# Kernel optimization log

Hardware: AMD Instinct MI355X
Metric: run time of the kernel (lower is better)

The kernel has to match this reference:

```python
import jax, jax.numpy as jnp
import numpy as np

N_SEQ, N_RES, C_M, C_Z, C, N_HEAD = 256, 256, 256, 128, 32, 8
EPS = 1e-5


def layernorm(x, w, b):
    mu = jnp.mean(x, axis=-1, keepdims=True)
    var = jnp.mean((x - mu) ** 2, axis=-1, keepdims=True)
    return (x - mu) * jax.lax.rsqrt(var + EPS) * w + b


def setup_inputs() -> dict:
    key = jax.random.key(0)
    ks = jax.random.split(key, 12)
    s = 0.02
    return {
        "m": jax.random.normal(ks[0], (N_SEQ, N_RES, C_M), jnp.float32),
        "z": jax.random.normal(ks[1], (N_RES, N_RES, C_Z), jnp.float32),
        "ln_m_w": jnp.ones((C_M,), jnp.float32),
        "ln_m_b": jnp.zeros((C_M,), jnp.float32),
        "ln_z_w": jnp.ones((C_Z,), jnp.float32),
        "ln_z_b": jnp.zeros((C_Z,), jnp.float32),
        "Wz": jax.random.normal(ks[2], (C_Z, N_HEAD), jnp.float32) * s,   # pair bias proj, no bias
        "Wq": jax.random.normal(ks[3], (C_M, N_HEAD * C), jnp.float32) * s,
        "Wk": jax.random.normal(ks[4], (C_M, N_HEAD * C), jnp.float32) * s,
        "Wv": jax.random.normal(ks[5], (C_M, N_HEAD * C), jnp.float32) * s,
        "Wg": jax.random.normal(ks[6], (C_M, N_HEAD * C), jnp.float32) * s,
        "bg": jnp.zeros((N_HEAD * C,), jnp.float32),
        "Wo": jax.random.normal(ks[7], (N_HEAD * C, C_M), jnp.float32) * s,
        "bo": jnp.zeros((C_M,), jnp.float32),
    }


def reference(m, z, ln_m_w, ln_m_b, ln_z_w, ln_z_b, Wz, Wq, Wk, Wv, Wg, bg, Wo, bo):
    # LayerNorm on msa and pair reps
    mn = layernorm(m, ln_m_w, ln_m_b)                       # (S, R, c_m)
    b = layernorm(z, ln_z_w, ln_z_b) @ Wz                    # (R, R, H)
    b = jnp.moveaxis(b, -1, -3)                              # (H, R, R)

    def proj(W):  # (S, R, H, C) -> (S, H, R, C)
        return (mn @ W).reshape(N_SEQ, N_RES, N_HEAD, C).transpose(0, 2, 1, 3)

    q = proj(Wq) / jnp.sqrt(jnp.float32(C))
    k = proj(Wk)
    v = proj(Wv)

    scores = jnp.einsum("shqc,shkc->shqk", q, k) + b         # bias broadcasts over S
    a = jax.nn.softmax(scores, axis=-1)
    o = jnp.einsum("shqk,shkc->shqc", a, v)                  # (S, H, R, C)
    o = o.transpose(0, 2, 1, 3).reshape(N_SEQ, N_RES, N_HEAD * C)

    g = jax.nn.sigmoid(mn @ Wg + bg)                          # gating
    return (g * o) @ Wo + bo                                  # (S, R, c_m)
```

## Files before the change

kernel.cpp:

```cpp
#include <hip/hip_runtime.h>
#include <stdint.h>

#define NSEQ 256
#define NRES 256
#define CM   256
#define CZ   128
#define CH   32
#define NHEAD 8
#define EPSF 1e-5f

typedef __bf16 bf16x8 __attribute__((ext_vector_type(8)));
typedef float  f32x4  __attribute__((ext_vector_type(4)));
typedef float  f32x16 __attribute__((ext_vector_type(16)));

__device__ __forceinline__ ushort f2bf(float f) {
    union { float f; uint32_t u; } v; v.f = f;
    uint32_t r = (v.u + 0x7FFFu + ((v.u >> 16) & 1u)) >> 16;
    return (ushort)r;
}
__device__ __forceinline__ float bf2f(ushort h) {
    union { uint32_t u; float f; } v; v.u = ((uint32_t)h) << 16;
    return v.f;
}
__device__ __forceinline__ float bfl(uint32_t u) {
    union { uint32_t x; float f; } v; v.x = u << 16; return v.f;
}
__device__ __forceinline__ float bfh(uint32_t u) {
    union { uint32_t x; float f; } v; v.x = u & 0xffff0000u; return v.f;
}
__device__ __forceinline__ unsigned int cvt_pk_bf16(float lo, float hi_) {
    unsigned int r;
    asm("v_cvt_pk_bf16_f32 %0, %1, %2" : "=v"(r) : "v"(lo), "v"(hi_));
    return r;
}

__device__ __forceinline__ void gload16(const void* g, void* l) {
    __builtin_amdgcn_global_load_lds(
        (const __attribute__((address_space(1))) void*)g,
        (__attribute__((address_space(3))) void*)l,
        16, 0, 0);
}

__global__ void prep_weights_kernel(const float* __restrict__ Wq,
                                    const float* __restrict__ Wk,
                                    const float* __restrict__ Wv,
                                    const float* __restrict__ Wg,
                                    const float* __restrict__ Wo,
                                    ushort* __restrict__ Wt,
                                    ushort* __restrict__ WoT) {
    int n = blockIdx.x;
    int k = threadIdx.x;
    if (n < 1024) {
        int nn = n & 255;
        const float* src;
        float scale = 1.0f;
        if      (n < 256) { src = Wq; scale = 0.17677669529663687f; }
        else if (n < 512) { src = Wk; }
        else if (n < 768) { src = Wv; }
        else              { src = Wg; }
        Wt[n * 256 + k] = f2bf(src[k * 256 + nn] * scale);
    } else {
        int nn = n - 1024;
        WoT[nn * 256 + k] = f2bf(Wo[k * 256 + nn]);
    }
}

__global__ __launch_bounds__(256) void ln_m_kernel(const float* __restrict__ m,
                                                   const float* __restrict__ w,
                                                   const float* __restrict__ b,
                                                   ushort* __restrict__ mn) {
    int gw   = (blockIdx.x * blockDim.x + threadIdx.x) >> 6;
    int lane = threadIdx.x & 63;
    const float* row = m + (size_t)gw * 256;
    float4 x = *(const float4*)(row + lane * 4);
    float s  = x.x + x.y + x.z + x.w;
    float sq = x.x * x.x + x.y * x.y + x.z * x.z + x.w * x.w;
#pragma unroll
    for (int off = 32; off; off >>= 1) {
        s  += __shfl_xor(s, off, 64);
        sq += __shfl_xor(sq, off, 64);
    }
    float mu  = s * (1.0f / 256.0f);
    float var = sq * (1.0f / 256.0f) - mu * mu;
    float rs  = rsqrtf(var + EPSF);
    float4 wv = *(const float4*)(w + lane * 4);
    float4 bv = *(const float4*)(b + lane * 4);
    ushort4 o;
    o.x = f2bf((x.x - mu) * rs * wv.x + bv.x);
    o.y = f2bf((x.y - mu) * rs * wv.y + bv.y);
    o.z = f2bf((x.z - mu) * rs * wv.z + bv.z);
    o.w = f2bf((x.w - mu) * rs * wv.w + bv.w);
    *(ushort4*)(mn + (size_t)gw * 256 + lane * 4) = o;
}

__global__ __launch_bounds__(256) void ln_z_bias_kernel(const float* __restrict__ z,
                                                        const float* __restrict__ w,
                                                        const float* __restrict__ b,
                                                        const float* __restrict__ Wz,
                                                        ushort* __restrict__ biasb) {
    int gw   = (blockIdx.x * blockDim.x + threadIdx.x) >> 6;
    int lane = threadIdx.x & 63;
    float wz0[8], wz1[8];
#pragma unroll
    for (int h = 0; h < 8; ++h) {
        wz0[h] = Wz[(2 * lane) * 8 + h];
        wz1[h] = Wz[(2 * lane + 1) * 8 + h];
    }
    float w0 = w[2 * lane], w1 = w[2 * lane + 1];
    float b0 = b[2 * lane], b1 = b[2 * lane + 1];
    for (int row = gw; row < 65536; row += 8192) {
        float2 x = *(const float2*)(z + (size_t)row * 128 + 2 * lane);
        float s = x.x + x.y, sq = x.x * x.x + x.y * x.y;
#pragma unroll
        for (int off = 32; off; off >>= 1) {
            s  += __shfl_xor(s, off, 64);
            sq += __shfl_xor(sq, off, 64);
        }
        float mu = s * (1.0f / 128.0f);
        float rs = rsqrtf(sq * (1.0f / 128.0f) - mu * mu + EPSF);
        float z0 = (x.x - mu) * rs * w0 + b0;
        float z1 = (x.y - mu) * rs * w1 + b1;
        float acc[8];
#pragma unroll
        for (int h = 0; h < 8; ++h) acc[h] = z0 * wz0[h] + z1 * wz1[h];
#pragma unroll
        for (int h = 0; h < 8; ++h)
#pragma unroll
            for (int off = 32; off; off >>= 1) acc[h] += __shfl_xor(acc[h], off, 64);
        if (lane < 8) {
            int jc = row & 31;
            int posv = ((jc & 4) << 2) | ((jc & 24) >> 1) | (jc & 3);
            biasb[lane * 65536 + (row & ~31) + posv] = f2bf(acc[lane]);
        }
    }
}

__global__ __launch_bounds__(256) void proj_gemm_kernel(const ushort* __restrict__ mn,
                                                        const ushort* __restrict__ Wt,
                                                        const float* __restrict__ bg,
                                                        ushort* __restrict__ Q,
                                                        ushort* __restrict__ K,
                                                        ushort* __restrict__ Vt,
                                                        ushort* __restrict__ G) {
    __shared__ ushort SH[32768];
    int bid = blockIdx.x;
    int wid = ((bid & 7) << 9) | (bid >> 3);
    int by = wid >> 3, bx = wid & 7;
    int m0 = by << 7, n0 = bx << 7;
    int t = threadIdx.x, lane = t & 63, w = t >> 6;
    int l15 = lane & 15, l4 = lane >> 4;
    int wr = w >> 1, wc = w & 1;

    int srow  = t >> 3;
    int scolh = (((lane & 7) ^ ((lane >> 3) & 7)) << 3);
    const ushort* Ag = mn + (size_t)(m0 + srow) * 256 + scolh;
    const ushort* Bg = Wt + (size_t)(n0 + srow) * 256 + scolh;

    auto stage = [&](int kt) {
        int k0 = kt << 6;
        int bufo = (kt & 1) << 14;
#pragma unroll
        for (int i = 0; i < 4; ++i) {
            gload16(Ag + (size_t)(i * 32) * 256 + k0, &SH[bufo + t * 8 + i * 2048]);
            gload16(Bg + (size_t)(i * 32) * 256 + k0, &SH[bufo + 8192 + t * 8 + i * 2048]);
        }
    };

    f32x4 acc[4][4] = {};
    stage(0);

    for (int kt = 0; kt < 4; ++kt) {
        __syncthreads();
        if (kt < 3) stage(kt + 1);
        int bufo = (kt & 1) << 14;
#pragma unroll
        for (int ks = 0; ks < 2; ++ks) {
            int xr = ks * 4 + l4;
            bf16x8 af[4], bfr[4];
#pragma unroll
            for (int mi = 0; mi < 4; ++mi) {
                int row = wr * 64 + mi * 16 + l15;
                af[mi] = *(const bf16x8*)&SH[bufo + row * 64 + ((xr ^ (l15 & 7)) << 3)];
            }
#pragma unroll
            for (int ni = 0; ni < 4; ++ni) {
                int row = wc * 64 + ni * 16 + l15;
                bfr[ni] = *(const bf16x8*)&SH[bufo + 8192 + row * 64 + ((xr ^ (l15 & 7)) << 3)];
            }
#pragma unroll
            for (int mi = 0; mi < 4; ++mi)
#pragma unroll
                for (int ni = 0; ni < 4; ++ni)
                    acc[mi][ni] = __builtin_amdgcn_mfma_f32_16x16x32_bf16(af[mi], bfr[ni], acc[mi][ni], 0, 0, 0);
        }
    }

    __syncthreads();

    int region = bx >> 1;
    int ss = m0 >> 8;

    if (region == 2) {
        int rbase = (m0 & 255) + wr * 64 + l4 * 4;
#pragma unroll
        for (int ni = 0; ni < 4; ++ni) {
            int nn = (n0 & 255) + wc * 64 + ni * 16 + l15;
            int h = nn >> 5, c = nn & 31;
#pragma unroll
            for (int mi = 0; mi < 4; ++mi) {
                int rr = rbase + mi * 16;
                ushort4 pv;
                pv.x = f2bf(acc[mi][ni][0]); pv.y = f2bf(acc[mi][ni][1]);
                pv.z = f2bf(acc[mi][ni][2]); pv.w = f2bf(acc[mi][ni][3]);
                *(ushort4*)&Vt[((size_t)(ss * 8 + h) * 32 + c) * 256 + rr] = pv;
            }
        }
    } else {
        ushort* E = SH + w * 1152;
        int base_nn = (bx & 1) * 128 + wc * 64;
        int rloc = lane >> 2, seg = lane & 3;
#pragma unroll
        for (int mi = 0; mi < 4; ++mi) {
            if (region == 3) {
#pragma unroll
                for (int ni = 0; ni < 4; ++ni) {
                    float bgv = bg[base_nn + ni * 16 + l15];
#pragma unroll
                    for (int r = 0; r < 4; ++r) {
                        float x = acc[mi][ni][r] + bgv;
                        E[(l4 * 4 + r) * 72 + ni * 16 + l15] =
                            f2bf(1.0f / (1.0f + __expf(-x)));
                    }
                }
            } else {
#pragma unroll
                for (int ni = 0; ni < 4; ++ni)
#pragma unroll
                    for (int r = 0; r < 4; ++r)
                        E[(l4 * 4 + r) * 72 + ni * 16 + l15] = f2bf(acc[mi][ni][r]);
            }
            uint4 v0 = *(const uint4*)&E[rloc * 72 + seg * 16];
            uint4 v1 = *(const uint4*)&E[rloc * 72 + seg * 16 + 8];
            int rr  = (m0 & 255) + wr * 64 + mi * 16 + rloc;
            int nn0 = base_nn + seg * 16;
            int h0 = nn0 >> 5, c0 = nn0 & 31;
            int nn1 = nn0 + 8;
            int h1 = nn1 >> 5, c1 = nn1 & 31;
            if (region <= 1) {
                ushort* dst = (region == 0) ? Q : K;
                *(uint4*)&dst[(size_t)(ss * 8 + h0) * 8192 + rr * 32 + c0] = v0;
                *(uint4*)&dst[(size_t)(ss * 8 + h1) * 8192 + rr * 32 + c1] = v1;
            } else {
                *(uint4*)&G[((size_t)h0 << 21) + (ss << 13) + (rr << 5) + c0] = v0;
                *(uint4*)&G[((size_t)h1 << 21) + (ss << 13) + (rr << 5) + c1] = v1;
            }
        }
    }
}

__global__ __launch_bounds__(512, 4) void attn_kernel(const ushort* __restrict__ Q,
                                                      const ushort* __restrict__ K,
                                                      const ushort* __restrict__ Vt,
                                                      const ushort* __restrict__ G,
                                                      const ushort* __restrict__ biasb,
                                                      ushort* __restrict__ GO) {
    __shared__ ushort smem[32768];
    const int t = threadIdx.x;
    const int lane = t & 63, w = t >> 6;
    const int l31 = lane & 31, hi = lane >> 5;
    const int h = blockIdx.x & 7, s0 = blockIdx.x >> 3;
    const int q0 = w * 32;

    auto stage = [&](int i) {
        size_t shb = (size_t)((i * 64 + s0) * 8 + h) * 8192;
        const ushort* Kg = K + shb;
        const ushort* Vg = Vt + shb;
        int bufo = (i & 1) * 16384;
#pragma unroll
        for (int rd = 0; rd < 2; ++rd) {
            int g1 = rd * 512 + t;
            int kk = g1 >> 2;
            int lgk = (g1 & 3) ^ ((kk >> 1) & 3);
            gload16(Kg + kk * 32 + lgk * 8, &smem[bufo + g1 * 8]);
            int cc = g1 >> 5;
            int lgv = (g1 & 31) ^ (cc & 7);
            gload16(Vg + cc * 256 + lgv * 8, &smem[bufo + 8192 + g1 * 8]);
        }
    };

    stage(0);

    for (int i = 0; i < 4; ++i) {
        __syncthreads();
        if (i < 3) stage(i + 1);

        const int s = i * 64 + s0;
        const size_t shb = (size_t)(s * 8 + h) * 8192;
        const int bufo = (i & 1) * 16384;

        bf16x8 qf0 = *(const bf16x8*)&Q[shb + (size_t)(q0 + l31) * 32 + hi * 8];
        bf16x8 qf1 = *(const bf16x8*)&Q[shb + (size_t)(q0 + l31) * 32 + 16 + hi * 8];

        const ushort* bp = biasb + (size_t)h * 65536 + (size_t)(q0 + l31) * 256 + hi * 16;
        const int vbase = bufo + 8192 + l31 * 256;
        const int vswz = l31 & 7;

        float l_run = 0.f;
        f32x16 oa = {}, ob = {};

#pragma unroll 2
        for (int kt = 0; kt < 8; ++kt) {
            uint4 b0 = *(const uint4*)&bp[kt * 32];
            uint4 b1 = *(const uint4*)&bp[kt * 32 + 8];
            f32x16 sa;
            sa[0]  = bfl(b0.x); sa[1]  = bfh(b0.x);
            sa[2]  = bfl(b0.y); sa[3]  = bfh(b0.y);
            sa[4]  = bfl(b0.z); sa[5]  = bfh(b0.z);
            sa[6]  = bfl(b0.w); sa[7]  = bfh(b0.w);
            sa[8]  = bfl(b1.x); sa[9]  = bfh(b1.x);
            sa[10] = bfl(b1.y); sa[11] = bfh(b1.y);
            sa[12] = bfl(b1.z); sa[13] = bfh(b1.z);
            sa[14] = bfl(b1.w); sa[15] = bfh(b1.w);

            int krow = kt * 32 + l31;
            int swz = (krow >> 1) & 3;
            int rb = bufo + krow * 32;
            bf16x8 kf0 = *(const bf16x8*)&smem[rb + ((hi ^ swz) << 3)];
            bf16x8 kf1 = *(const bf16x8*)&smem[rb + (((2 + hi) ^ swz) << 3)];
            sa = __builtin_amdgcn_mfma_f32_32x32x16_bf16(kf0, qf0, sa, 0, 0, 0);
            sa = __builtin_amdgcn_mfma_f32_32x32x16_bf16(kf1, qf1, sa, 0, 0, 0);

            float ls0 = 0.f, ls1 = 0.f;
#pragma unroll
            for (int r = 0; r < 16; r += 2) {
                float p0 = __expf(sa[r]);
                float p1 = __expf(sa[r + 1]);
                sa[r] = p0; sa[r + 1] = p1;
                ls0 += p0; ls1 += p1;
            }
            l_run += ls0 + ls1;

            unsigned int w0[4], w1[4];
#pragma unroll
            for (int mm = 0; mm < 4; ++mm) {
                w0[mm] = cvt_pk_bf16(sa[4 * mm + 0], sa[4 * mm + 1]);
                w1[mm] = cvt_pk_bf16(sa[4 * mm + 2], sa[4 * mm + 3]);
            }
#pragma unroll
            for (int hh = 0; hh < 2; ++hh) {
                unsigned int F0 = w0[2 * hh], H0 = w0[2 * hh + 1];
                unsigned int F1 = w1[2 * hh], H1 = w1[2 * hh + 1];
                asm("v_permlane32_swap_b32 %0, %1" : "+v"(F0), "+v"(H0));
                asm("v_permlane32_swap_b32 %0, %1" : "+v"(F1), "+v"(H1));
                uint4 fw = make_uint4(F0, F1, H0, H1);
                bf16x8 pf = *(bf16x8*)&fw;
                int g = kt * 4 + hh * 2 + hi;
                bf16x8 vf = *(const bf16x8*)&smem[vbase + ((g ^ vswz) << 3)];
                if (hh) ob = __builtin_amdgcn_mfma_f32_32x32x16_bf16(vf, pf, ob, 0, 0, 0);
                else    oa = __builtin_amdgcn_mfma_f32_32x32x16_bf16(vf, pf, oa, 0, 0, 0);
            }
        }

        l_run += __shfl_xor(l_run, 32, 64);
        float rinv = 1.0f / l_run;

        const size_t grow = ((size_t)h << 21) + ((size_t)s << 13) + ((q0 + l31) << 5) + hi * 4;
#pragma unroll
        for (int g = 0; g < 4; ++g) {
            ushort4 gv = *(const ushort4*)&G[grow + g * 8];
            float o0 = (oa[4 * g + 0] + ob[4 * g + 0]) * rinv * bf2f(gv.x);
            float o1 = (oa[4 * g + 1] + ob[4 * g + 1]) * rinv * bf2f(gv.y);
            float o2 = (oa[4 * g + 2] + ob[4 * g + 2]) * rinv * bf2f(gv.z);
            float o3 = (oa[4 * g + 3] + ob[4 * g + 3]) * rinv * bf2f(gv.w);
            ushort4 ov;
            ov.x = f2bf(o0); ov.y = f2bf(o1); ov.z = f2bf(o2); ov.w = f2bf(o3);
            *(ushort4*)&GO[grow + g * 8] = ov;
        }
    }
}

__global__ __launch_bounds__(256) void out_gemm_kernel(const ushort* __restrict__ GO,
                                                       const ushort* __restrict__ WoT,
                                                       const float* __restrict__ bo,
                                                       float* __restrict__ out) {
    __shared__ ushort SH[32768];
    int bid = blockIdx.x;
    int wid = ((bid & 7) << 7) | (bid >> 3);
    int by = wid >> 1, bx = wid & 1;
    int m0 = by << 7, n0 = bx << 7;
    int t = threadIdx.x, lane = t & 63, w = t >> 6;
    int l15 = lane & 15, l4 = lane >> 4;
    int wr = w >> 1, wc = w & 1;

    int srow  = t >> 3;
    int scolh = (((lane & 7) ^ ((lane >> 3) & 7)) << 3);
    const ushort* Ag = GO + ((size_t)(scolh >> 5) << 21) + ((size_t)(m0 + srow) << 5) + (scolh & 31);
    const ushort* Bg = WoT + (size_t)(n0 + srow) * 256 + scolh;

    auto stage = [&](int kt) {
        int k0 = kt << 6;
        int bufo = (kt & 1) << 14;
#pragma unroll
        for (int i = 0; i < 4; ++i) {
            gload16(Ag + ((size_t)kt << 22) + (i << 10), &SH[bufo + t * 8 + i * 2048]);
            gload16(Bg + (size_t)(i * 32) * 256 + k0, &SH[bufo + 8192 + t * 8 + i * 2048]);
        }
    };

    f32x4 acc[4][4] = {};
    stage(0);

    for (int kt = 0; kt < 4; ++kt) {
        __syncthreads();
        if (kt < 3) stage(kt + 1);
        int bufo = (kt & 1) << 14;
#pragma unroll
        for (int ks = 0; ks < 2; ++ks) {
            int xr = ks * 4 + l4;
            bf16x8 af[4], bfr[4];
#pragma unroll
            for (int mi = 0; mi < 4; ++mi) {
                int row = wr * 64 + mi * 16 + l15;
                af[mi] = *(const bf16x8*)&SH[bufo + row * 64 + ((xr ^ (l15 & 7)) << 3)];
            }
#pragma unroll
            for (int ni = 0; ni < 4; ++ni) {
                int row = wc * 64 + ni * 16 + l15;
                bfr[ni] = *(const bf16x8*)&SH[bufo + 8192 + row * 64 + ((xr ^ (l15 & 7)) << 3)];
            }
#pragma unroll
            for (int mi = 0; mi < 4; ++mi)
#pragma unroll
                for (int ni = 0; ni < 4; ++ni)
                    acc[mi][ni] = __builtin_amdgcn_mfma_f32_16x16x32_bf16(af[mi], bfr[ni], acc[mi][ni], 0, 0, 0);
        }
    }

    int crow0 = m0 + wr * 64 + l4 * 4;
#pragma unroll
    for (int ni = 0; ni < 4; ++ni) {
        int col = n0 + wc * 64 + ni * 16 + l15;
        float bov = bo[col];
#pragma unroll
        for (int mi = 0; mi < 4; ++mi)
#pragma unroll
            for (int r = 0; r < 4; ++r)
                out[(size_t)(crow0 + mi * 16 + r) * 256 + col] = acc[mi][ni][r] + bov;
    }
}

extern "C" void kernel_launch(void* const* d_in, const int* in_sizes, int n_in,
                              void* d_out, int out_size, void* d_ws, size_t ws_size,
                              hipStream_t stream) {
    const float* m      = (const float*)d_in[0];
    const float* z      = (const float*)d_in[1];
    const float* ln_m_w = (const float*)d_in[2];
    const float* ln_m_b = (const float*)d_in[3];
    const float* ln_z_w = (const float*)d_in[4];
    const float* ln_z_b = (const float*)d_in[5];
    const float* Wz     = (const float*)d_in[6];
    const float* Wq     = (const float*)d_in[7];
    const float* Wk     = (const float*)d_in[8];
    const float* Wv     = (const float*)d_in[9];
    const float* Wg     = (const float*)d_in[10];
    const float* bg     = (const float*)d_in[11];
    const float* Wo     = (const float*)d_in[12];
    const float* bo     = (const float*)d_in[13];
    float* out = (float*)d_out;

    char* ws = (char*)d_ws;
    ushort* Wt    = (ushort*)(ws + 0);
    ushort* WoT   = (ushort*)(ws + 524288);
    ushort* biasb = (ushort*)(ws + 655360);
    ushort* mn    = (ushort*)(ws + 2752512);
    ushort* GO    = mn;
    ushort* Q     = (ushort*)(ws + 36306944);
    ushort* K     = (ushort*)(ws + 69861376);
    ushort* Vt    = (ushort*)(ws + 103415808);
    ushort* G     = (ushort*)(ws + 136970240);

    prep_weights_kernel<<<1280, 256, 0, stream>>>(Wq, Wk, Wv, Wg, Wo, Wt, WoT);
    ln_m_kernel<<<16384, 256, 0, stream>>>(m, ln_m_w, ln_m_b, mn);
    ln_z_bias_kernel<<<2048, 256, 0, stream>>>(z, ln_z_w, ln_z_b, Wz, biasb);
    proj_gemm_kernel<<<4096, 256, 0, stream>>>(mn, Wt, bg, Q, K, Vt, G);
    attn_kernel<<<512, 512, 0, stream>>>(Q, K, Vt, G, biasb, GO);
    out_gemm_kernel<<<1024, 256, 0, stream>>>(GO, WoT, bo, out);
}
```

Before: 227.6 us.

## Merge preprocessing kernels, use butterfly bias reduction, shrink GEMM K-tile for occupancy

Three preprocessing kernels (weight transpose, m LayerNorm, z LayerNorm plus bias projection) are merged into one launch that dispatches on block index, which removes launch gaps. The 8-head bias reduction now uses a transpose-style butterfly shuffle, so each lane ends up holding one head, instead of 8 full cross-lane reductions. The projection GEMM K-tile is halved from 64 to 32, which halves LDS per block and adds a launch bound of 4 for occupancy. In exchange it needs twice as many barrier iterations, and the LDS swizzle and head index mapping are new and could introduce errors.

```diff
diff --git a/kernel.cpp b/kernel.cpp
--- a/kernel.cpp
+++ b/kernel.cpp
@@ -41,108 +41,127 @@
         16, 0, 0);
 }
 
-__global__ void prep_weights_kernel(const float* __restrict__ Wq,
-                                    const float* __restrict__ Wk,
-                                    const float* __restrict__ Wv,
-                                    const float* __restrict__ Wg,
-                                    const float* __restrict__ Wo,
-                                    ushort* __restrict__ Wt,
-                                    ushort* __restrict__ WoT) {
-    int n = blockIdx.x;
-    int k = threadIdx.x;
-    if (n < 1024) {
-        int nn = n & 255;
-        const float* src;
-        float scale = 1.0f;
-        if      (n < 256) { src = Wq; scale = 0.17677669529663687f; }
-        else if (n < 512) { src = Wk; }
-        else if (n < 768) { src = Wv; }
-        else              { src = Wg; }
-        Wt[n * 256 + k] = f2bf(src[k * 256 + nn] * scale);
-    } else {
-        int nn = n - 1024;
-        WoT[nn * 256 + k] = f2bf(Wo[k * 256 + nn]);
-    }
-}
-
-__global__ __launch_bounds__(256) void ln_m_kernel(const float* __restrict__ m,
-                                                   const float* __restrict__ w,
-                                                   const float* __restrict__ b,
-                                                   ushort* __restrict__ mn) {
-    int gw   = (blockIdx.x * blockDim.x + threadIdx.x) >> 6;
-    int lane = threadIdx.x & 63;
-    const float* row = m + (size_t)gw * 256;
-    float4 x = *(const float4*)(row + lane * 4);
-    float s  = x.x + x.y + x.z + x.w;
-    float sq = x.x * x.x + x.y * x.y + x.z * x.z + x.w * x.w;
-#pragma unroll
-    for (int off = 32; off; off >>= 1) {
-        s  += __shfl_xor(s, off, 64);
-        sq += __shfl_xor(sq, off, 64);
-    }
-    float mu  = s * (1.0f / 256.0f);
-    float var = sq * (1.0f / 256.0f) - mu * mu;
-    float rs  = rsqrtf(var + EPSF);
-    float4 wv = *(const float4*)(w + lane * 4);
-    float4 bv = *(const float4*)(b + lane * 4);
-    ushort4 o;
-    o.x = f2bf((x.x - mu) * rs * wv.x + bv.x);
-    o.y = f2bf((x.y - mu) * rs * wv.y + bv.y);
-    o.z = f2bf((x.z - mu) * rs * wv.z + bv.z);
-    o.w = f2bf((x.w - mu) * rs * wv.w + bv.w);
-    *(ushort4*)(mn + (size_t)gw * 256 + lane * 4) = o;
-}
-
-__global__ __launch_bounds__(256) void ln_z_bias_kernel(const float* __restrict__ z,
-                                                        const float* __restrict__ w,
-                                                        const float* __restrict__ b,
-                                                        const float* __restrict__ Wz,
-                                                        ushort* __restrict__ biasb) {
-    int gw   = (blockIdx.x * blockDim.x + threadIdx.x) >> 6;
-    int lane = threadIdx.x & 63;
-    float wz0[8], wz1[8];
-#pragma unroll
-    for (int h = 0; h < 8; ++h) {
-        wz0[h] = Wz[(2 * lane) * 8 + h];
-        wz1[h] = Wz[(2 * lane + 1) * 8 + h];
-    }
-    float w0 = w[2 * lane], w1 = w[2 * lane + 1];
-    float b0 = b[2 * lane], b1 = b[2 * lane + 1];
-    for (int row = gw; row < 65536; row += 8192) {
-        float2 x = *(const float2*)(z + (size_t)row * 128 + 2 * lane);
-        float s = x.x + x.y, sq = x.x * x.x + x.y * x.y;
+__global__ __launch_bounds__(256) void pre_kernel(const float* __restrict__ m,
+                                                  const float* __restrict__ ln_m_w,
+                                                  const float* __restrict__ ln_m_b,
+                                                  const float* __restrict__ z,
+                                                  const float* __restrict__ ln_z_w,
+                                                  const float* __restrict__ ln_z_b,
+                                                  const float* __restrict__ Wz,
+                                                  const float* __restrict__ Wq,
+                                                  const float* __restrict__ Wk,
+                                                  const float* __restrict__ Wv,
+                                                  const float* __restrict__ Wg,
+                                                  const float* __restrict__ Wo,
+                                                  ushort* __restrict__ mn,
+                                                  ushort* __restrict__ biasb,
+                                                  ushort* __restrict__ Wt,
+                                                  ushort* __restrict__ WoT) {
+    int b = blockIdx.x;
+    int t = threadIdx.x;
+    int lane = t & 63;
+
+    if (b < 16384) {
+        int gw = (b * 256 + t) >> 6;
+        const float* row = m + (size_t)gw * 256;
+        float4 x = *(const float4*)(row + lane * 4);
+        float s  = x.x + x.y + x.z + x.w;
+        float sq = x.x * x.x + x.y * x.y + x.z * x.z + x.w * x.w;
 #pragma unroll
         for (int off = 32; off; off >>= 1) {
             s  += __shfl_xor(s, off, 64);
             sq += __shfl_xor(sq, off, 64);
         }
-        float mu = s * (1.0f / 128.0f);
-        float rs = rsqrtf(sq * (1.0f / 128.0f) - mu * mu + EPSF);
-        float z0 = (x.x - mu) * rs * w0 + b0;
-        float z1 = (x.y - mu) * rs * w1 + b1;
-        float acc[8];
-#pragma unroll
-        for (int h = 0; h < 8; ++h) acc[h] = z0 * wz0[h] + z1 * wz1[h];
-#pragma unroll
-        for (int h = 0; h < 8; ++h)
-#pragma unroll
-            for (int off = 32; off; off >>= 1) acc[h] += __shfl_xor(acc[h], off, 64);
-        if (lane < 8) {
-            int jc = row & 31;
-            int posv = ((jc & 4) << 2) | ((jc & 24) >> 1) | (jc & 3);
-            biasb[lane * 65536 + (row & ~31) + posv] = f2bf(acc[lane]);
+        float mu  = s * (1.0f / 256.0f);
+        float var = sq * (1.0f / 256.0f) - mu * mu;
+        float rs  = rsqrtf(var + EPSF);
+        float4 wv = *(const float4*)(ln_m_w + lane * 4);
+        float4 bv = *(const float4*)(ln_m_b + lane * 4);
+        ushort4 o;
+        o.x = f2bf((x.x - mu) * rs * wv.x + bv.x);
+        o.y = f2bf((x.y - mu) * rs * wv.y + bv.y);
+        o.z = f2bf((x.z - mu) * rs * wv.z + bv.z);
+        o.w = f2bf((x.w - mu) * rs * wv.w + bv.w);
+        *(ushort4*)(mn + (size_t)gw * 256 + lane * 4) = o;
+    } else if (b < 18432) {
+        int gw = ((b - 16384) * 256 + t) >> 6;
+        float wz0[8], wz1[8];
+#pragma unroll
+        for (int h = 0; h < 8; ++h) {
+            wz0[h] = Wz[(2 * lane) * 8 + h];
+            wz1[h] = Wz[(2 * lane + 1) * 8 + h];
+        }
+        float w0 = ln_z_w[2 * lane], w1 = ln_z_w[2 * lane + 1];
+        float b0 = ln_z_b[2 * lane], b1 = ln_z_b[2 * lane + 1];
+        for (int row = gw; row < 65536; row += 8192) {
+            float2 x = *(const float2*)(z + (size_t)row * 128 + 2 * lane);
+            float s = x.x + x.y, sq = x.x * x.x + x.y * x.y;
+#pragma unroll
+            for (int off = 32; off; off >>= 1) {
+                s  += __shfl_xor(s, off, 64);
+                sq += __shfl_xor(sq, off, 64);
+            }
+            float mu = s * (1.0f / 128.0f);
+            float rs = rsqrtf(sq * (1.0f / 128.0f) - mu * mu + EPSF);
+            float z0 = (x.x - mu) * rs * w0 + b0;
+            float z1 = (x.y - mu) * rs * w1 + b1;
+            float acc[8];
+#pragma unroll
+            for (int h = 0; h < 8; ++h) acc[h] = z0 * wz0[h] + z1 * wz1[h];
+            float u[4];
+#pragma unroll
+            for (int i = 0; i < 4; ++i) {
+                float send = (lane & 1) ? acc[i] : acc[i + 4];
+                float rec  = __shfl_xor(send, 1, 64);
+                u[i] = ((lane & 1) ? acc[i + 4] : acc[i]) + rec;
+            }
+            float v2[2];
+#pragma unroll
+            for (int i = 0; i < 2; ++i) {
+                float send = (lane & 2) ? u[i] : u[i + 2];
+                float rec  = __shfl_xor(send, 2, 64);
+                v2[i] = ((lane & 2) ? u[i + 2] : u[i]) + rec;
+            }
+            float send = (lane & 4) ? v2[0] : v2[1];
+            float rec  = __shfl_xor(send, 4, 64);
+            float vv = ((lane & 4) ? v2[1] : v2[0]) + rec;
+            vv += __shfl_xor(vv, 8, 64);
+            vv += __shfl_xor(vv, 16, 64);
+            vv += __shfl_xor(vv, 32, 64);
+            if (lane < 8) {
+                int hh = ((lane & 1) << 2) | (lane & 2) | ((lane >> 2) & 1);
+                int jc = row & 31;
+                int posv = ((jc & 4) << 2) | ((jc & 24) >> 1) | (jc & 3);
+                biasb[hh * 65536 + (row & ~31) + posv] = f2bf(vv);
+            }
+        }
+    } else {
+        int n = b - 18432;
+        int k = t;
+        if (n < 1024) {
+            int nn = n & 255;
+            const float* src;
+            float scale = 1.0f;
+            if      (n < 256) { src = Wq; scale = 0.17677669529663687f; }
+            else if (n < 512) { src = Wk; }
+            else if (n < 768) { src = Wv; }
+            else              { src = Wg; }
+            Wt[n * 256 + k] = f2bf(src[k * 256 + nn] * scale);
+        } else {
+            int nn = n - 1024;
+            WoT[nn * 256 + k] = f2bf(Wo[k * 256 + nn]);
         }
     }
 }
 
-__global__ __launch_bounds__(256) void proj_gemm_kernel(const ushort* __restrict__ mn,
-                                                        const ushort* __restrict__ Wt,
-                                                        const float* __restrict__ bg,
-                                                        ushort* __restrict__ Q,
-                                                        ushort* __restrict__ K,
-                                                        ushort* __restrict__ Vt,
-                                                        ushort* __restrict__ G) {
-    __shared__ ushort SH[32768];
+__global__ __launch_bounds__(256, 4) void proj_gemm_kernel(const ushort* __restrict__ mn,
+                                                           const ushort* __restrict__ Wt,
+                                                           const float* __restrict__ bg,
+                                                           ushort* __restrict__ Q,
+                                                           ushort* __restrict__ K,
+                                                           ushort* __restrict__ Vt,
+                                                           ushort* __restrict__ G) {
+    __shared__ ushort SH[16384];
     int bid = blockIdx.x;
     int wid = ((bid & 7) << 9) | (bid >> 3);
     int by = wid >> 3, bx = wid & 7;
@@ -151,48 +170,46 @@
     int l15 = lane & 15, l4 = lane >> 4;
     int wr = w >> 1, wc = w & 1;
 
-    int srow  = t >> 3;
-    int scolh = (((lane & 7) ^ ((lane >> 3) & 7)) << 3);
-    const ushort* Ag = mn + (size_t)(m0 + srow) * 256 + scolh;
-    const ushort* Bg = Wt + (size_t)(n0 + srow) * 256 + scolh;
+    int srow  = t >> 2;
+    int sgran = t & 3;
+    int scol  = (sgran ^ (srow & 3)) << 3;
+    const ushort* Ag = mn + (size_t)(m0 + srow) * 256 + scol;
+    const ushort* Bg = Wt + (size_t)(n0 + srow) * 256 + scol;
 
     auto stage = [&](int kt) {
-        int k0 = kt << 6;
-        int bufo = (kt & 1) << 14;
-#pragma unroll
-        for (int i = 0; i < 4; ++i) {
-            gload16(Ag + (size_t)(i * 32) * 256 + k0, &SH[bufo + t * 8 + i * 2048]);
-            gload16(Bg + (size_t)(i * 32) * 256 + k0, &SH[bufo + 8192 + t * 8 + i * 2048]);
-        }
+        int k0 = kt << 5;
+        int bufo = (kt & 1) << 13;
+        gload16(Ag + k0,             &SH[bufo + t * 8]);
+        gload16(Ag + 64 * 256 + k0,  &SH[bufo + 2048 + t * 8]);
+        gload16(Bg + k0,             &SH[bufo + 4096 + t * 8]);
+        gload16(Bg + 64 * 256 + k0,  &SH[bufo + 4096 + 2048 + t * 8]);
     };
 
     f32x4 acc[4][4] = {};
     stage(0);
 
-    for (int kt = 0; kt < 4; ++kt) {
+    int rg = (l4 ^ (l15 & 3)) << 3;
+
+    for (int kt = 0; kt < 8; ++kt) {
         __syncthreads();
-        if (kt < 3) stage(kt + 1);
-        int bufo = (kt & 1) << 14;
-#pragma unroll
-        for (int ks = 0; ks < 2; ++ks) {
-            int xr = ks * 4 + l4;
-            bf16x8 af[4], bfr[4];
-#pragma unroll
-            for (int mi = 0; mi < 4; ++mi) {
-                int row = wr * 64 + mi * 16 + l15;
-                af[mi] = *(const bf16x8*)&SH[bufo + row * 64 + ((xr ^ (l15 & 7)) << 3)];
-            }
-#pragma unroll
-            for (int ni = 0; ni < 4; ++ni) {
-                int row = wc * 64 + ni * 16 + l15;
-                bfr[ni] = *(const bf16x8*)&SH[bufo + 8192 + row * 64 + ((xr ^ (l15 & 7)) << 3)];
-            }
-#pragma unroll
-            for (int mi = 0; mi < 4; ++mi)
-#pragma unroll
-                for (int ni = 0; ni < 4; ++ni)
-                    acc[mi][ni] = __builtin_amdgcn_mfma_f32_16x16x32_bf16(af[mi], bfr[ni], acc[mi][ni], 0, 0, 0);
-        }
+        if (kt < 7) stage(kt + 1);
+        int bufo = (kt & 1) << 13;
+        bf16x8 af[4], bfr[4];
+#pragma unroll
+        for (int mi = 0; mi < 4; ++mi) {
+            int row = wr * 64 + mi * 16 + l15;
+            af[mi] = *(const bf16x8*)&SH[bufo + row * 32 + rg];
+        }
+#pragma unroll
+        for (int ni = 0; ni < 4; ++ni) {
+            int row = wc * 64 + ni * 16 + l15;
+            bfr[ni] = *(const bf16x8*)&SH[bufo + 4096 + row * 32 + rg];
+        }
+#pragma unroll
+        for (int mi = 0; mi < 4; ++mi)
+#pragma unroll
+            for (int ni = 0; ni < 4; ++ni)
+                acc[mi][ni] = __builtin_amdgcn_mfma_f32_16x16x32_bf16(af[mi], bfr[ni], acc[mi][ni], 0, 0, 0);
     }
 
     __syncthreads();
@@ -479,9 +496,9 @@
     ushort* Vt    = (ushort*)(ws + 103415808);
     ushort* G     = (ushort*)(ws + 136970240);
 
-    prep_weights_kernel<<<1280, 256, 0, stream>>>(Wq, Wk, Wv, Wg, Wo, Wt, WoT);
-    ln_m_kernel<<<16384, 256, 0, stream>>>(m, ln_m_w, ln_m_b, mn);
-    ln_z_bias_kernel<<<2048, 256, 0, stream>>>(z, ln_z_w, ln_z_b, Wz, biasb);
+    pre_kernel<<<19712, 256, 0, stream>>>(m, ln_m_w, ln_m_b, z, ln_z_w, ln_z_b,
+                                          Wz, Wq, Wk, Wv, Wg, Wo,
+                                          mn, biasb, Wt, WoT);
     proj_gemm_kernel<<<4096, 256, 0, stream>>>(mn, Wt, bg, Q, K, Vt, G);
     attn_kernel<<<512, 512, 0, stream>>>(Q, K, Vt, G, biasb, GO);
     out_gemm_kernel<<<1024, 256, 0, stream>>>(GO, WoT, bo, out);
```

Result: faster. 190.9 us (-16.1%).
